# Kernel tuning notes

Hardware: AMD Instinct MI355X
Metric: run time of the kernel (lower is better)

The kernel has to match this reference:

```python
import jax, jax.numpy as jnp
import numpy as np

B = 128          # batch size
N_KG = 500       # KG vertices
N = N_KG + 2     # + sensor node + zero target node
D = 1024         # embed_dim (hard-coded in forward)
H = 256          # gnn_hidden
E = 4000         # edges
EPS = 1e-5


def setup_inputs() -> dict:
    key = jax.random.key(0)
    ks = jax.random.split(key, 8)
    return {
        "sensor_batch": jax.random.normal(ks[0], (B, D), jnp.float32),
        "base_vertices": jax.random.normal(ks[1], (N_KG, D), jnp.float32),
        "edge_index": jax.random.randint(ks[2], (2, E), 0, N, jnp.int64),
        "W1": jax.random.normal(ks[3], (D, H), jnp.float32) * (1.0 / np.sqrt(D)),
        "b1": jnp.zeros((H,), jnp.float32),
        "gamma1": jnp.ones((H,), jnp.float32),
        "beta1": jnp.zeros((H,), jnp.float32),
        "W2": jax.random.normal(ks[4], (H, H), jnp.float32) * (1.0 / np.sqrt(H)),
        "b2": jnp.zeros((H,), jnp.float32),
        "gamma2": jnp.ones((H,), jnp.float32),
        "beta2": jnp.zeros((H,), jnp.float32),
        "W3": jax.random.normal(ks[5], (H, H), jnp.float32) * (1.0 / np.sqrt(H)),
        "b3": jnp.zeros((H,), jnp.float32),
        "gamma3": jnp.ones((H,), jnp.float32),
        "beta3": jnp.zeros((H,), jnp.float32),
    }


def _gcn_norm(edge_index):
    # add self loops, symmetric normalization D^{-1/2} A D^{-1/2}
    loops = jnp.arange(N, dtype=edge_index.dtype)
    src = jnp.concatenate([edge_index[0], loops])
    dst = jnp.concatenate([edge_index[1], loops])
    deg = jnp.zeros((N,), jnp.float32).at[dst].add(1.0)
    dinv = jnp.where(deg > 0, jax.lax.rsqrt(deg), 0.0)
    norm = dinv[src] * dinv[dst]   # [E+N]
    return src, dst, norm


def _gcn_conv(x, W, b, src, dst, norm):
    # x: [B, N, F_in] -> [B, N, F_out]
    h = jnp.einsum('bnf,fh->bnh', x, W)
    msg = h[:, src, :] * norm[None, :, None]            # gather + scale
    out = jnp.zeros_like(h).at[:, dst, :].add(msg)      # scatter-add
    return out + b


def _bn_elu(x, gamma, beta):
    # BatchNorm1d over flattened (B*N, H) in training mode, then ELU
    Bn, Nn, Hh = x.shape
    xf = x.reshape(Bn * Nn, Hh)
    mean = jnp.mean(xf, axis=0)
    var = jnp.mean(jnp.square(xf - mean), axis=0)  # biased, as in torch BN fwd
    y = (xf - mean) * jax.lax.rsqrt(var + EPS) * gamma + beta
    return jax.nn.elu(y).reshape(Bn, Nn, Hh)


def reference(sensor_batch, base_vertices, edge_index,
              W1, b1, gamma1, beta1,
              W2, b2, gamma2, beta2,
              W3, b3, gamma3, beta3):
    Bn = sensor_batch.shape[0]
    # x = [base_vertices; sensor_input; zeros] per batch element -> [B, N, D]
    base = jnp.broadcast_to(base_vertices[None], (Bn, N_KG, D))
    zeros = jnp.zeros((Bn, 1, D), sensor_batch.dtype)
    x = jnp.concatenate([base, sensor_batch[:, None, :], zeros], axis=1)

    src, dst, norm = _gcn_norm(edge_index)
    x = _bn_elu(_gcn_conv(x, W1, b1, src, dst, norm), gamma1, beta1)
    x = _bn_elu(_gcn_conv(x, W2, b2, src, dst, norm), gamma2, beta2)
    x = _bn_elu(_gcn_conv(x, W3, b3, src, dst, norm), gamma3, beta3)
    return x
```

## Files before the change

kernel.cpp:

```cpp
#include <hip/hip_runtime.h>
#include <cstdint>
#include <cstddef>

#define NNODES 502
#define NKG    500
#define NPAD   512
#define NEDGE  4000
#define NET    4502
#define BB     128
#define DD     1024
#define HH     256
#define MROWS  (BB*NNODES)
#define MT     65536
#define MCAT   628

typedef short short8 __attribute__((ext_vector_type(8)));
typedef float f32x4  __attribute__((ext_vector_type(4)));

__device__ __forceinline__ unsigned short f2bf(float f) {
  union { float f; unsigned int u; } v; v.f = f;
  unsigned int r = v.u + 0x7fffu + ((v.u >> 16) & 1u);
  return (unsigned short)(r >> 16);
}

__device__ __forceinline__ float bf2f(unsigned short u) {
  union { unsigned int u; float f; } v; v.u = ((unsigned int)u) << 16;
  return v.f;
}

__device__ __forceinline__ float elu(float y) {
  return (y > 0.f) ? y : (__expf(y) - 1.f);
}

__device__ __forceinline__ void stage16(const void* g, void* l) {
  __builtin_amdgcn_global_load_lds((__attribute__((address_space(1))) void*)g,
                                   (__attribute__((address_space(3))) void*)l, 16, 0, 0);
}

__device__ __forceinline__ void mfma16(f32x4& c, short8 a, short8 b) {
  asm volatile("v_mfma_f32_16x16x32_bf16 %0, %1, %2, %0" : "+v"(c) : "v"(a), "v"(b));
}

__device__ inline void get_edge(const int* __restrict__ e, int i, int i64mode,
                                int& src, int& dst) {
  if (i < NEDGE) {
    if (i64mode) { src = e[2*i]; dst = e[2*NEDGE + 2*i]; }
    else         { src = e[i];   dst = e[NEDGE + i]; }
  } else {
    src = dst = i - NEDGE;
  }
  src = min(max(src, 0), NNODES-1);
  dst = min(max(dst, 0), NNODES-1);
}

__global__ void detect_kernel(const int* __restrict__ e, int* __restrict__ flag) {
  int v = e[2*threadIdx.x + 1];
  if (v != 0) atomicOr(flag, 1);
}

__global__ void deg_kernel(const int* __restrict__ e, const int* __restrict__ flag,
                           int* __restrict__ deg) {
  int i = blockIdx.x*256 + threadIdx.x;
  if (i >= NET) return;
  int src, dst; get_edge(e, i, *flag == 0, src, dst);
  atomicAdd(&deg[dst], 1);
}

__global__ void scan_kernel(const int* __restrict__ deg, float* __restrict__ dinv,
                            int* __restrict__ rp, int* __restrict__ cursor) {
  __shared__ int s[512];
  int t = threadIdx.x;
  int cnt = (t < NNODES) ? deg[t] : 0;
  s[t] = cnt;
  if (t < NNODES) dinv[t] = rsqrtf((float)cnt);
  __syncthreads();
  for (int off = 1; off < 512; off <<= 1) {
    int v = (t >= off) ? s[t-off] : 0;
    __syncthreads();
    s[t] += v;
    __syncthreads();
  }
  if (t == 0) rp[0] = 0;
  if (t < NNODES) { rp[t+1] = s[t]; cursor[t] = s[t] - cnt; }
}

__global__ void fill_kernel(const int* __restrict__ e, const int* __restrict__ flag,
                            const float* __restrict__ dinv, int* __restrict__ cursor,
                            int* __restrict__ colA, float* __restrict__ valA) {
  int i = blockIdx.x*256 + threadIdx.x;
  if (i >= NET) return;
  int src, dst; get_edge(e, i, *flag == 0, src, dst);
  int pos = atomicAdd(&cursor[dst], 1);
  colA[pos] = src;
  valA[pos] = dinv[src] * dinv[dst];
}

__global__ void sdf_kernel(const int* __restrict__ e, const int* __restrict__ flag,
                           const float* __restrict__ dinv, float* __restrict__ Sdf) {
  int i = blockIdx.x*256 + threadIdx.x;
  if (i >= NET) return;
  int src, dst; get_edge(e, i, *flag == 0, src, dst);
  atomicAdd(&Sdf[dst*NPAD + src], dinv[src]*dinv[dst]);
}

__global__ void sdcvt_kernel(const float* __restrict__ Sdf, unsigned short* __restrict__ Sd) {
  int i = blockIdx.x*256 + threadIdx.x;
  Sd[i] = f2bf(Sdf[i]);
}

__global__ __launch_bounds__(256) void prep_kernel(
    const float* __restrict__ W1, const float* __restrict__ W2, const float* __restrict__ W3,
    const float* __restrict__ base, const float* __restrict__ sensor,
    unsigned short* __restrict__ Wt1, unsigned short* __restrict__ Wt2,
    unsigned short* __restrict__ Wt3, unsigned short* __restrict__ Xp1) {
  int bid = blockIdx.x, tid = threadIdx.x;
  if (bid < 512) {
    const float* W = (bid & 256) ? W3 : W2;
    unsigned short* Wt = (bid & 256) ? Wt3 : Wt2;
    int n = bid & 255;
    Wt[n*HH + tid] = f2bf(W[(size_t)tid*HH + n]);
  } else if (bid < 768) {
    int n = bid - 512;
    for (int k = tid; k < DD; k += 256)
      Wt1[n*DD + k] = f2bf(W1[(size_t)k*HH + n]);
  } else {
    int i = (bid - 768)*256 + tid;
    int r = i >> 8, c = (i & 255) * 4;
    float4 v = make_float4(0.f, 0.f, 0.f, 0.f);
    if (r < NKG) v = *(const float4*)&base[(size_t)r*DD + c];
    else if (r < MCAT) v = *(const float4*)&sensor[(size_t)(r-NKG)*DD + c];
    union { unsigned short u[4]; uint2 d; } p;
    p.u[0]=f2bf(v.x); p.u[1]=f2bf(v.y); p.u[2]=f2bf(v.z); p.u[3]=f2bf(v.w);
    *(uint2*)&Xp1[(size_t)r*DD + c] = p.d;
  }
}

__global__ __launch_bounds__(256) void gemm1m_kernel(
    const unsigned short* __restrict__ Ag,
    const unsigned short* __restrict__ Bg,
    float* __restrict__ C) {
  __shared__ unsigned short As[128*32];
  __shared__ unsigned short Bs[128*32];
  int tid = threadIdx.x;
  int wave = tid >> 6, lane = tid & 63;
  int l15 = lane & 15, quad = lane >> 4;
  int wm = (wave & 1) * 64, wn = (wave >> 1) * 64;
  int row0 = blockIdx.y * 128, col0 = blockIdx.x * 128;
  f32x4 acc[4][4] = {};
  for (int k0 = 0; k0 < DD; k0 += 32) {
#pragma unroll
    for (int q = 0; q < 2; ++q) {
      int c = wave*128 + q*64 + lane;
      stage16(Ag + (size_t)(row0 + (c>>2))*DD + k0 + (c&3)*8, As + c*8);
      stage16(Bg + (size_t)(col0 + (c>>2))*DD + k0 + (c&3)*8, Bs + c*8);
    }
    __syncthreads();
    short8 af[4], bfv[4];
#pragma unroll
    for (int i = 0; i < 4; ++i) {
      af[i]  = *(const short8*)(As + (wm + i*16 + l15)*32 + quad*8);
      bfv[i] = *(const short8*)(Bs + (wn + i*16 + l15)*32 + quad*8);
    }
#pragma unroll
    for (int mi = 0; mi < 4; ++mi)
#pragma unroll
      for (int ni = 0; ni < 4; ++ni)
        mfma16(acc[mi][ni], af[mi], bfv[ni]);
    __syncthreads();
  }
  asm volatile("s_nop 7\n\ts_nop 7" ::);
#pragma unroll
  for (int ni = 0; ni < 4; ++ni) {
    int n = col0 + wn + ni*16 + l15;
#pragma unroll
    for (int mi = 0; mi < 4; ++mi) {
      int m = row0 + wm + mi*16 + quad*4;
#pragma unroll
      for (int r = 0; r < 4; ++r)
        if (m + r < MCAT) C[(size_t)(m+r)*HH + n] = acc[mi][ni][r];
    }
  }
}

__global__ void ac_kernel(const int* __restrict__ rp, const int* __restrict__ colA,
                          const float* __restrict__ valA, const float* __restrict__ hcat,
                          float* __restrict__ Abuf, float* __restrict__ cbuf) {
  int n = blockIdx.x, h = threadIdx.x;
  int s = rp[n], e = rp[n+1];
  float acc = 0.f, cacc = 0.f;
  for (int t = s; t < e; ++t) {
    int cl = colA[t]; float v = valA[t];
    if (cl < NKG) acc += v * hcat[cl*HH + h];
    else if (cl == NKG) cacc += v;
  }
  Abuf[n*HH + h] = acc;
  if (h == 0) cbuf[n] = cacc;
}

__global__ __launch_bounds__(256) void bn1n_kernel(
    const float* __restrict__ Abuf, const float* __restrict__ cbuf,
    const float* __restrict__ hcat,
    float* __restrict__ sA1, float* __restrict__ sAA1, float* __restrict__ sAc1,
    float* __restrict__ scp, float* __restrict__ ssA, float* __restrict__ sssA) {
  int bid = blockIdx.x, h = threadIdx.x;
  if (bid < 32) {
    int n0 = bid*16, n1 = min(n0+16, NNODES);
    float sA = 0, sAA = 0, sAc = 0, sc = 0, scc = 0;
    for (int n = n0; n < n1; ++n) {
      float a = Abuf[n*HH + h]; float cn = cbuf[n];
      sA += a; sAA += a*a; sAc += a*cn; sc += cn; scc += cn*cn;
    }
    atomicAdd(&sA1[h], sA); atomicAdd(&sAA1[h], sAA); atomicAdd(&sAc1[h], sAc);
    if (h == 0) { atomicAdd(&scp[0], sc); atomicAdd(&scp[1], scc); }
  } else {
    int b0 = (bid-32)*16;
    float ss = 0, sss = 0;
    for (int b = b0; b < b0+16; ++b) {
      float v = hcat[(size_t)(NKG + b)*HH + h]; ss += v; sss += v*v;
    }
    atomicAdd(&ssA[h], ss); atomicAdd(&sssA[h], sss);
  }
}

__global__ void fin1_kernel(const float* __restrict__ sA1, const float* __restrict__ sAA1,
                            const float* __restrict__ sAc1, const float* __restrict__ scp,
                            const float* __restrict__ ssA, const float* __restrict__ sssA,
                            const float* __restrict__ gamma, const float* __restrict__ beta,
                            float* __restrict__ scale, float* __restrict__ shift) {
  int h = threadIdx.x;
  float sA = sA1[h], sAA = sAA1[h], sAc = sAc1[h];
  float sc = scp[0], scc = scp[1];
  float ss = ssA[h], sss = sssA[h];
  const float cnt = (float)MROWS;
  float mean = ((float)BB * sA + sc*ss) / cnt;
  float msq  = ((float)BB * sAA + 2.f*sAc*ss + scc*sss) / cnt;
  float var  = msq - mean*mean;
  float scl  = gamma[h] * rsqrtf(var + 1e-5f);
  scale[h] = scl; shift[h] = beta[h] - mean*scl;
}

__global__ __launch_bounds__(256) void x2_kernel(
    const float* __restrict__ Abuf, const float* __restrict__ cbuf,
    const float* __restrict__ hcat, const float* __restrict__ scale,
    const float* __restrict__ shift, unsigned short* __restrict__ Xb) {
  int idx = blockIdx.x*256 + threadIdx.x;
  int row = idx >> 6, h0 = (idx & 63)*4;
  int b = row >> 9, n = row & (NPAD-1);
  union { unsigned short u[4]; uint2 d; } p;
  p.d = make_uint2(0,0);
  if (n < NNODES) {
    float4 a  = *(const float4*)(Abuf + n*HH + h0);
    float4 s  = *(const float4*)(hcat + (size_t)(NKG + b)*HH + h0);
    float4 sc = *(const float4*)(scale + h0);
    float4 sh = *(const float4*)(shift + h0);
    float cn = cbuf[n];
    p.u[0] = f2bf(elu((a.x + cn*s.x)*sc.x + sh.x));
    p.u[1] = f2bf(elu((a.y + cn*s.y)*sc.y + sh.y));
    p.u[2] = f2bf(elu((a.z + cn*s.z)*sc.z + sh.z));
    p.u[3] = f2bf(elu((a.w + cn*s.w)*sc.w + sh.w));
  }
  *(uint2*)(Xb + (size_t)row*HH + h0) = p.d;
}

__global__ __launch_bounds__(256) void gemmT_kernel(
    const unsigned short* __restrict__ Ag,
    const unsigned short* __restrict__ Bg,
    unsigned short* __restrict__ Tt) {
  __shared__ unsigned short As[128*32];
  __shared__ unsigned short Bs[128*32];
  int tid = threadIdx.x;
  int wave = tid >> 6, lane = tid & 63;
  int l15 = lane & 15, quad = lane >> 4;
  int wm = (wave & 1) * 64, wn = (wave >> 1) * 64;
  int row0 = blockIdx.y * 128, col0 = blockIdx.x * 128;
  f32x4 acc[4][4] = {};
  for (int k0 = 0; k0 < HH; k0 += 32) {
#pragma unroll
    for (int q = 0; q < 2; ++q) {
      int c = wave*128 + q*64 + lane;
      stage16(Ag + (size_t)(row0 + (c>>2))*HH + k0 + (c&3)*8, As + c*8);
      stage16(Bg + (size_t)(col0 + (c>>2))*HH + k0 + (c&3)*8, Bs + c*8);
    }
    __syncthreads();
    short8 af[4], bfv[4];
#pragma unroll
    for (int i = 0; i < 4; ++i) {
      af[i]  = *(const short8*)(As + (wm + i*16 + l15)*32 + quad*8);
      bfv[i] = *(const short8*)(Bs + (wn + i*16 + l15)*32 + quad*8);
    }
#pragma unroll
    for (int mi = 0; mi < 4; ++mi)
#pragma unroll
      for (int ni = 0; ni < 4; ++ni)
        mfma16(acc[mi][ni], af[mi], bfv[ni]);
    __syncthreads();
  }
  asm volatile("s_nop 7\n\ts_nop 7" ::);
#pragma unroll
  for (int ni = 0; ni < 4; ++ni) {
    int n = col0 + wn + ni*16 + l15;
#pragma unroll
    for (int mi = 0; mi < 4; ++mi) {
      int m = row0 + wm + mi*16 + quad*4;
      union { unsigned short u[4]; uint2 v; } p;
#pragma unroll
      for (int r = 0; r < 4; ++r) p.u[r] = f2bf(acc[mi][ni][r]);
      *(uint2*)(Tt + (size_t)n*MT + m) = p.v;
    }
  }
}

__global__ __launch_bounds__(256) void gemmS_kernel(
    const unsigned short* __restrict__ Sd,
    const unsigned short* __restrict__ Tt,
    unsigned short* __restrict__ Xbo,
    float* __restrict__ sums, float* __restrict__ ssqs) {
  __shared__ unsigned short As[128*32];
  __shared__ unsigned short Bs[128*32];
  int tid = threadIdx.x;
  int wave = tid >> 6, lane = tid & 63;
  int l15 = lane & 15, quad = lane >> 4;
  int wm = (wave & 1) * 64, wn = (wave >> 1) * 64;
  int id = blockIdx.x;
  int xcd = id & 7;
  int w = id >> 3;
  int y = w & 3;
  int g = (w >> 2) * 8 + xcd;
  int x = g >> 7;
  int b = g & 127;
  int row0 = y * 128, col0 = x * 128;
  f32x4 acc[4][4] = {};
  for (int k0 = 0; k0 < NPAD; k0 += 32) {
#pragma unroll
    for (int q = 0; q < 2; ++q) {
      int c = wave*128 + q*64 + lane;
      stage16(Sd + (size_t)(row0 + (c>>2))*NPAD + k0 + (c&3)*8, As + c*8);
      stage16(Tt + (size_t)(col0 + (c>>2))*MT + b*NPAD + k0 + (c&3)*8, Bs + c*8);
    }
    __syncthreads();
    short8 af[4], bfv[4];
#pragma unroll
    for (int i = 0; i < 4; ++i) {
      af[i]  = *(const short8*)(As + (wm + i*16 + l15)*32 + quad*8);
      bfv[i] = *(const short8*)(Bs + (wn + i*16 + l15)*32 + quad*8);
    }
#pragma unroll
    for (int mi = 0; mi < 4; ++mi)
#pragma unroll
      for (int ni = 0; ni < 4; ++ni)
        mfma16(acc[mi][ni], af[mi], bfv[ni]);
    __syncthreads();
  }
  asm volatile("s_nop 7\n\ts_nop 7" ::);
  unsigned short* Xrow = Xbo + (size_t)b*NPAD*HH;
  float ps[4] = {0,0,0,0}, pq[4] = {0,0,0,0};
#pragma unroll
  for (int ni = 0; ni < 4; ++ni) {
    int n = col0 + wn + ni*16 + l15;
#pragma unroll
    for (int mi = 0; mi < 4; ++mi) {
      int node = row0 + wm + mi*16 + quad*4;
#pragma unroll
      for (int r = 0; r < 4; ++r) {
        float v = acc[mi][ni][r];
        if (node + r < NNODES) Xrow[(size_t)(node+r)*HH + n] = f2bf(v);
        ps[ni] += v; pq[ni] += v*v;
      }
    }
  }
  __syncthreads();
  float* red = (float*)As;
  red[tid] = 0.f;
  __syncthreads();
#pragma unroll
  for (int ni = 0; ni < 4; ++ni) {
    int cl = wn + ni*16 + l15;
    atomicAdd(&red[cl], ps[ni]);
    atomicAdd(&red[128+cl], pq[ni]);
  }
  __syncthreads();
  if (tid < 128) atomicAdd(&sums[col0+tid], red[tid]);
  else atomicAdd(&ssqs[col0+tid-128], red[tid]);
}

__global__ void finalize_kernel(const float* __restrict__ sums, const float* __restrict__ ssqs,
                                const float* __restrict__ gamma, const float* __restrict__ beta,
                                float* __restrict__ scale, float* __restrict__ shift) {
  int h = threadIdx.x;
  const float cnt = (float)MROWS;
  float mean = sums[h] / cnt;
  float var  = ssqs[h] / cnt - mean*mean;
  float scl  = gamma[h] * rsqrtf(var + 1e-5f);
  scale[h] = scl; shift[h] = beta[h] - mean*scl;
}

__global__ __launch_bounds__(256) void bnip_kernel(
    unsigned short* __restrict__ Xb, const float* __restrict__ scale,
    const float* __restrict__ shift) {
  int idx = blockIdx.x*256 + threadIdx.x;
  int row = idx >> 6, h0 = (idx & 63)*4;
  int n = row & (NPAD-1);
  if (n >= NNODES) return;
  unsigned short* p = Xb + (size_t)row*HH + h0;
  union { unsigned short u[4]; uint2 d; } v;
  v.d = *(uint2*)p;
  float4 sc = *(const float4*)(scale + h0);
  float4 sh = *(const float4*)(shift + h0);
  v.u[0] = f2bf(elu(bf2f(v.u[0])*sc.x + sh.x));
  v.u[1] = f2bf(elu(bf2f(v.u[1])*sc.y + sh.y));
  v.u[2] = f2bf(elu(bf2f(v.u[2])*sc.z + sh.z));
  v.u[3] = f2bf(elu(bf2f(v.u[3])*sc.w + sh.w));
  *(uint2*)p = v.d;
}

__global__ __launch_bounds__(256) void bnout_kernel(
    const unsigned short* __restrict__ Xb, const float* __restrict__ scale,
    const float* __restrict__ shift, float* __restrict__ O) {
  int idx = blockIdx.x*256 + threadIdx.x;
  int row = idx >> 6, h0 = (idx & 63)*4;
  int b = row >> 9, n = row & (NPAD-1);
  if (n >= NNODES) return;
  union { unsigned short u[4]; uint2 d; } v;
  v.d = *(const uint2*)(Xb + (size_t)row*HH + h0);
  float4 sc = *(const float4*)(scale + h0);
  float4 sh = *(const float4*)(shift + h0);
  float4 o;
  o.x = elu(bf2f(v.u[0])*sc.x + sh.x);
  o.y = elu(bf2f(v.u[1])*sc.y + sh.y);
  o.z = elu(bf2f(v.u[2])*sc.z + sh.z);
  o.w = elu(bf2f(v.u[3])*sc.w + sh.w);
  *(float4*)(O + ((size_t)(b*NNODES + n)*HH + h0)) = o;
}

extern "C" void kernel_launch(void* const* d_in, const int* in_sizes, int n_in,
                              void* d_out, int out_size, void* d_ws, size_t ws_size,
                              hipStream_t stream) {
  const float* sensor = (const float*)d_in[0];
  const float* base   = (const float*)d_in[1];
  const int*   eidx   = (const int*)d_in[2];
  const float* W1 = (const float*)d_in[3];
  const float* g1 = (const float*)d_in[5];
  const float* be1= (const float*)d_in[6];
  const float* W2 = (const float*)d_in[7];
  const float* g2 = (const float*)d_in[9];
  const float* be2= (const float*)d_in[10];
  const float* W3 = (const float*)d_in[11];
  const float* g3 = (const float*)d_in[13];
  const float* be3= (const float*)d_in[14];

  char* ws = (char*)d_ws;
  int*   deg    = (int*)(ws + 0);
  float* sum2   = (float*)(ws + 2048);
  float* ssq2   = (float*)(ws + 3072);
  float* sum3   = (float*)(ws + 4096);
  float* ssq3   = (float*)(ws + 5120);
  float* cbuf   = (float*)(ws + 6144);
  int*   cursor = (int*)(ws + 8192);
  int*   flag   = (int*)(ws + 10240);
  float* sA1    = (float*)(ws + 10496);
  float* sAA1   = (float*)(ws + 11520);
  float* sAc1   = (float*)(ws + 12544);
  float* scp    = (float*)(ws + 13568);
  float* ssA    = (float*)(ws + 13824);
  float* sssA   = (float*)(ws + 14848);
  float* dinv   = (float*)(ws + 16384);
  int*   rp     = (int*)(ws + 18432);
  int*   colA   = (int*)(ws + 20480);
  float* valA   = (float*)(ws + 40960);
  float* scale1 = (float*)(ws + 61440);
  float* shift1 = (float*)(ws + 62464);
  float* scale2 = (float*)(ws + 63488);
  float* shift2 = (float*)(ws + 64512);
  float* scale3 = (float*)(ws + 65536);
  float* shift3 = (float*)(ws + 66560);
  float* Abuf   = (float*)(ws + 67584);
  float* hcat   = (float*)(ws + 581632);
  unsigned short* Wt2 = (unsigned short*)(ws + 1224704);
  unsigned short* Wt3 = (unsigned short*)(ws + 1355776);
  unsigned short* Sd  = (unsigned short*)(ws + 1486848);
  unsigned short* Xb  = (unsigned short*)(ws + 2011136);
  unsigned short* Tt  = (unsigned short*)(ws + 35565568UL);
  unsigned short* Xp1 = (unsigned short*)(ws + 35565568UL);
  unsigned short* Wt1 = (unsigned short*)(ws + 35565568UL + 1310720);
  float* out = (float*)d_out;
  float* Sdf = (float*)d_out;

  hipMemsetAsync(ws, 0, 16384, stream);
  hipMemsetAsync(d_out, 0, NPAD*NPAD*4, stream);
  detect_kernel<<<1, 256, 0, stream>>>(eidx, flag);
  deg_kernel<<<(NET+255)/256, 256, 0, stream>>>(eidx, flag, deg);
  scan_kernel<<<1, 512, 0, stream>>>(deg, dinv, rp, cursor);
  fill_kernel<<<(NET+255)/256, 256, 0, stream>>>(eidx, flag, dinv, cursor, colA, valA);
  sdf_kernel<<<(NET+255)/256, 256, 0, stream>>>(eidx, flag, dinv, Sdf);
  sdcvt_kernel<<<(NPAD*NPAD)/256, 256, 0, stream>>>(Sdf, Sd);
  prep_kernel<<<1408, 256, 0, stream>>>(W1, W2, W3, base, sensor, Wt1, Wt2, Wt3, Xp1);

  gemm1m_kernel<<<dim3(2, 5), 256, 0, stream>>>(Xp1, Wt1, hcat);
  ac_kernel<<<NNODES, 256, 0, stream>>>(rp, colA, valA, hcat, Abuf, cbuf);
  bn1n_kernel<<<40, 256, 0, stream>>>(Abuf, cbuf, hcat, sA1, sAA1, sAc1, scp, ssA, sssA);
  fin1_kernel<<<1, 256, 0, stream>>>(sA1, sAA1, sAc1, scp, ssA, sssA, g1, be1, scale1, shift1);
  x2_kernel<<<(MT*64)/256, 256, 0, stream>>>(Abuf, cbuf, hcat, scale1, shift1, Xb);

  gemmT_kernel<<<dim3(2, MT/128), 256, 0, stream>>>(Xb, Wt2, Tt);
  gemmS_kernel<<<1024, 256, 0, stream>>>(Sd, Tt, Xb, sum2, ssq2);
  finalize_kernel<<<1, 256, 0, stream>>>(sum2, ssq2, g2, be2, scale2, shift2);
  bnip_kernel<<<(MT*64)/256, 256, 0, stream>>>(Xb, scale2, shift2);

  gemmT_kernel<<<dim3(2, MT/128), 256, 0, stream>>>(Xb, Wt3, Tt);
  gemmS_kernel<<<1024, 256, 0, stream>>>(Sd, Tt, Xb, sum3, ssq3);
  finalize_kernel<<<1, 256, 0, stream>>>(sum3, ssq3, g3, be3, scale3, shift3);
  bnout_kernel<<<(MT*64)/256, 256, 0, stream>>>(Xb, scale3, shift3, out);
}
```

Before: 328.8 us.

## Double K-step per barrier and stage GEMM epilogues through LDS for wide stores

Both GEMM kernels now load a 64-wide K slice per iteration, two 32-wide halves into a larger shared buffer, which halves the number of barrier pairs. The epilogues write bf16 results into a padded shared tile first and then emit coalesced 16-byte global stores. Previously the T kernel did scattered 8-byte stores with a large stride and the S kernel did 2-byte scattered stores. In exchange each block uses more LDS, which may lower occupancy, and the epilogue needs extra barriers.

New measurement: 325.9 us. About the same (-0.9%).

```diff
diff --git a/kernel.cpp b/kernel.cpp
--- a/kernel.cpp
+++ b/kernel.cpp
@@ -13,6 +13,7 @@
 #define MROWS  (BB*NNODES)
 #define MT     65536
 #define MCAT   628
+#define EPITCH 136
 
 typedef short short8 __attribute__((ext_vector_type(8)));
 typedef float f32x4  __attribute__((ext_vector_type(4)));
@@ -266,47 +267,59 @@
     const unsigned short* __restrict__ Ag,
     const unsigned short* __restrict__ Bg,
     unsigned short* __restrict__ Tt) {
-  __shared__ unsigned short As[128*32];
-  __shared__ unsigned short Bs[128*32];
+  __shared__ __align__(16) unsigned short smem[128*EPITCH];
+  unsigned short* As = smem;
+  unsigned short* Bs = smem + 8192;
   int tid = threadIdx.x;
   int wave = tid >> 6, lane = tid & 63;
   int l15 = lane & 15, quad = lane >> 4;
   int wm = (wave & 1) * 64, wn = (wave >> 1) * 64;
   int row0 = blockIdx.y * 128, col0 = blockIdx.x * 128;
   f32x4 acc[4][4] = {};
-  for (int k0 = 0; k0 < HH; k0 += 32) {
-#pragma unroll
-    for (int q = 0; q < 2; ++q) {
-      int c = wave*128 + q*64 + lane;
-      stage16(Ag + (size_t)(row0 + (c>>2))*HH + k0 + (c&3)*8, As + c*8);
-      stage16(Bg + (size_t)(col0 + (c>>2))*HH + k0 + (c&3)*8, Bs + c*8);
-    }
-    __syncthreads();
-    short8 af[4], bfv[4];
-#pragma unroll
-    for (int i = 0; i < 4; ++i) {
-      af[i]  = *(const short8*)(As + (wm + i*16 + l15)*32 + quad*8);
-      bfv[i] = *(const short8*)(Bs + (wn + i*16 + l15)*32 + quad*8);
-    }
-#pragma unroll
-    for (int mi = 0; mi < 4; ++mi)
-#pragma unroll
-      for (int ni = 0; ni < 4; ++ni)
-        mfma16(acc[mi][ni], af[mi], bfv[ni]);
+  for (int k0 = 0; k0 < HH; k0 += 64) {
+#pragma unroll
+    for (int q = 0; q < 4; ++q) {
+      int c = q*256 + wave*64 + lane;
+      int half = c >> 9, rr = (c >> 2) & 127, j = c & 3;
+      stage16(Ag + (size_t)(row0 + rr)*HH + k0 + half*32 + j*8, As + c*8);
+      stage16(Bg + (size_t)(col0 + rr)*HH + k0 + half*32 + j*8, Bs + c*8);
+    }
+    __syncthreads();
+#pragma unroll
+    for (int kb = 0; kb < 2; ++kb) {
+      short8 af[4], bfv[4];
+#pragma unroll
+      for (int i = 0; i < 4; ++i) {
+        af[i]  = *(const short8*)(As + kb*4096 + (wm + i*16 + l15)*32 + quad*8);
+        bfv[i] = *(const short8*)(Bs + kb*4096 + (wn + i*16 + l15)*32 + quad*8);
+      }
+#pragma unroll
+      for (int mi = 0; mi < 4; ++mi)
+#pragma unroll
+        for (int ni = 0; ni < 4; ++ni)
+          mfma16(acc[mi][ni], af[mi], bfv[ni]);
+    }
     __syncthreads();
   }
   asm volatile("s_nop 7\n\ts_nop 7" ::);
 #pragma unroll
   for (int ni = 0; ni < 4; ++ni) {
-    int n = col0 + wn + ni*16 + l15;
+    int nl = wn + ni*16 + l15;
 #pragma unroll
     for (int mi = 0; mi < 4; ++mi) {
-      int m = row0 + wm + mi*16 + quad*4;
-      union { unsigned short u[4]; uint2 v; } p;
-#pragma unroll
-      for (int r = 0; r < 4; ++r) p.u[r] = f2bf(acc[mi][ni][r]);
-      *(uint2*)(Tt + (size_t)n*MT + m) = p.v;
-    }
+      int ml = wm + mi*16 + quad*4;
+#pragma unroll
+      for (int r = 0; r < 4; ++r)
+        smem[nl*EPITCH + ml + r] = f2bf(acc[mi][ni][r]);
+    }
+  }
+  __syncthreads();
+  int moff = (tid & 15)*8;
+#pragma unroll
+  for (int j = 0; j < 8; ++j) {
+    int nr = (tid >> 4) + j*16;
+    uint4 d = *(const uint4*)(smem + nr*EPITCH + moff);
+    *(uint4*)(Tt + (size_t)(col0 + nr)*MT + row0 + moff) = d;
   }
 }
 
@@ -315,8 +328,9 @@
     const unsigned short* __restrict__ Tt,
     unsigned short* __restrict__ Xbo,
     float* __restrict__ sums, float* __restrict__ ssqs) {
-  __shared__ unsigned short As[128*32];
-  __shared__ unsigned short Bs[128*32];
+  __shared__ __align__(16) unsigned short smem[128*EPITCH];
+  unsigned short* As = smem;
+  unsigned short* Bs = smem + 8192;
   int tid = threadIdx.x;
   int wave = tid >> 6, lane = tid & 63;
   int l15 = lane & 15, quad = lane >> 4;
@@ -330,46 +344,67 @@
   int b = g & 127;
   int row0 = y * 128, col0 = x * 128;
   f32x4 acc[4][4] = {};
-  for (int k0 = 0; k0 < NPAD; k0 += 32) {
-#pragma unroll
-    for (int q = 0; q < 2; ++q) {
-      int c = wave*128 + q*64 + lane;
-      stage16(Sd + (size_t)(row0 + (c>>2))*NPAD + k0 + (c&3)*8, As + c*8);
-      stage16(Tt + (size_t)(col0 + (c>>2))*MT + b*NPAD + k0 + (c&3)*8, Bs + c*8);
-    }
-    __syncthreads();
-    short8 af[4], bfv[4];
-#pragma unroll
-    for (int i = 0; i < 4; ++i) {
-      af[i]  = *(const short8*)(As + (wm + i*16 + l15)*32 + quad*8);
-      bfv[i] = *(const short8*)(Bs + (wn + i*16 + l15)*32 + quad*8);
-    }
+  for (int k0 = 0; k0 < NPAD; k0 += 64) {
+#pragma unroll
+    for (int q = 0; q < 4; ++q) {
+      int c = q*256 + wave*64 + lane;
+      int half = c >> 9, rr = (c >> 2) & 127, j = c & 3;
+      stage16(Sd + (size_t)(row0 + rr)*NPAD + k0 + half*32 + j*8, As + c*8);
+      stage16(Tt + (size_t)(col0 + rr)*MT + b*NPAD + k0 + half*32 + j*8, Bs + c*8);
+    }
+    __syncthreads();
+#pragma unroll
+    for (int kb = 0; kb < 2; ++kb) {
+      short8 af[4], bfv[4];
+#pragma unroll
+      for (int i = 0; i < 4; ++i) {
+        af[i]  = *(const short8*)(As + kb*4096 + (wm + i*16 + l15)*32 + quad*8);
+        bfv[i] = *(const short8*)(Bs + kb*4096 + (wn + i*16 + l15)*32 + quad*8);
+      }
+#pragma unroll
+      for (int mi = 0; mi < 4; ++mi)
+#pragma unroll
+        for (int ni = 0; ni < 4; ++ni)
+          mfma16(acc[mi][ni], af[mi], bfv[ni]);
+    }
+    __syncthreads();
+  }
+  asm volatile("s_nop 7\n\ts_nop 7" ::);
+  float ps[4] = {0,0,0,0}, pq[4] = {0,0,0,0};
+#pragma unroll
+  for (int ni = 0; ni < 4; ++ni)
 #pragma unroll
     for (int mi = 0; mi < 4; ++mi)
-#pragma unroll
-      for (int ni = 0; ni < 4; ++ni)
-        mfma16(acc[mi][ni], af[mi], bfv[ni]);
-    __syncthreads();
-  }
-  asm volatile("s_nop 7\n\ts_nop 7" ::);
-  unsigned short* Xrow = Xbo + (size_t)b*NPAD*HH;
-  float ps[4] = {0,0,0,0}, pq[4] = {0,0,0,0};
-#pragma unroll
-  for (int ni = 0; ni < 4; ++ni) {
-    int n = col0 + wn + ni*16 + l15;
-#pragma unroll
-    for (int mi = 0; mi < 4; ++mi) {
-      int node = row0 + wm + mi*16 + quad*4;
 #pragma unroll
       for (int r = 0; r < 4; ++r) {
         float v = acc[mi][ni][r];
-        if (node + r < NNODES) Xrow[(size_t)(node+r)*HH + n] = f2bf(v);
         ps[ni] += v; pq[ni] += v*v;
       }
+#pragma unroll
+  for (int mi = 0; mi < 4; ++mi) {
+    int ml = wm + mi*16 + quad*4;
+#pragma unroll
+    for (int ni = 0; ni < 4; ++ni) {
+      int nl = wn + ni*16 + l15;
+#pragma unroll
+      for (int r = 0; r < 4; ++r)
+        smem[(ml + r)*EPITCH + nl] = f2bf(acc[mi][ni][r]);
     }
   }
   __syncthreads();
-  float* red = (float*)As;
+  unsigned short* Xrow = Xbo + (size_t)b*NPAD*HH;
+  int noff = (tid & 15)*8;
+#pragma unroll
+  for (int j = 0; j < 8; ++j) {
+    int rr = (tid >> 4) + j*16;
+    int node = row0 + rr;
+    if (node < NNODES) {
+      uint4 d = *(const uint4*)(smem + rr*EPITCH + noff);
+      *(uint4*)(Xrow + (size_t)node*HH + col0 + noff) = d;
+    }
+  }
+  __syncthreads();
+  float* red = (float*)smem;
   red[tid] = 0.f;
   __syncthreads();
 #pragma unroll
```
